# Performance work log

Measured on AMD Instinct MI355X. Metric: run time of the kernel, lower is better.

The kernel has to match this reference:

```python
import jax, jax.numpy as jnp
import numpy as np

HEADS = 8
NEG = -1e9
EPS = 1e-9


def setup_inputs() -> dict:
    key = jax.random.key(0)
    ks = jax.random.split(key, 24)
    N, D, E = 2048, 512, 64
    s = 0.02
    inp = {
        "xyz": jax.random.normal(ks[0], (N, 3), jnp.float32),
        "str_feat": jax.random.normal(ks[1], (N, D), jnp.float32),
        "esm_feat": jax.random.normal(ks[2], (N, E), jnp.float32),
        "y_hat": jax.random.uniform(ks[3], (N, 1), jnp.float32),
        "distance_mask": jax.random.randint(ks[4], (N, N), 0, 2, jnp.int32),
        "t": jnp.ones((1,), jnp.float32),
        "band_width": jnp.ones((1,), jnp.float32),
        "max_iter": 5,
        # main projections (torch Linear layout: y = x @ W.T + b)
        "Wq": jax.random.normal(ks[5], (D, D), jnp.float32) * s,
        "bq": jnp.zeros((D,), jnp.float32),
        "Wk": jax.random.normal(ks[6], (D, D), jnp.float32) * s,
        "bk": jnp.zeros((D,), jnp.float32),
        "Wv": jax.random.normal(ks[7], (D, D), jnp.float32) * s,
        "bv": jnp.zeros((D,), jnp.float32),
        "Wo": jax.random.normal(ks[8], (D, D), jnp.float32) * s,
        "bo": jnp.zeros((D,), jnp.float32),
        # esm projections (computed in the original forward but unused downstream)
        "Weq": jax.random.normal(ks[9], (E, E), jnp.float32) * s,
        "beq": jnp.zeros((E,), jnp.float32),
        "Wek": jax.random.normal(ks[10], (E, E), jnp.float32) * s,
        "bek": jnp.zeros((E,), jnp.float32),
        "Wev": jax.random.normal(ks[11], (E, E), jnp.float32) * s,
        "bev": jnp.zeros((E,), jnp.float32),
        "Weo": jax.random.normal(ks[12], (E, E), jnp.float32) * s,
        "beo": jnp.zeros((E,), jnp.float32),
    }
    return inp


def reference(xyz, str_feat, esm_feat, y_hat, distance_mask, t, band_width, max_iter,
              Wq, bq, Wk, bk, Wv, bv, Wo, bo,
              Weq, beq, Wek, bek, Wev, bev, Weo, beo):
    N, D = str_feat.shape
    h = HEADS
    dh = D // h

    q = str_feat @ Wq.T + bq
    k = str_feat @ Wk.T + bk
    v = str_feat @ Wv.T + bv
    # esm projections: computed in the original forward but never used (dead code; DCE'd under jit)
    _esm_q = esm_feat @ Weq.T + beq
    _esm_k = esm_feat @ Wek.T + bek
    _esm_v = esm_feat @ Wev.T + bev

    # [h, N, dh]
    qh = q.reshape(N, h, dh).transpose(1, 0, 2)
    kh = k.reshape(N, h, dh).transpose(1, 0, 2)
    vh = v.reshape(N, h, dh).transpose(1, 0, 2)

    scores = jnp.einsum('hnd,hmd->hnm', qh, kh) / jnp.sqrt(jnp.asarray(dh, qh.dtype))
    mask = (distance_mask > 0)[None]              # [1, N, N]
    yw = y_hat[:, 0][None, :]                     # [1, N] per-target weight
    inv_two_bw2 = 1.0 / (2.0 * band_width[0] ** 2)
    temp = t[0]

    def step(carry, _):
        xyz_c, _x = carry
        # squared pairwise distances via the expanded form (avoids [N,N,3])
        sq = jnp.sum(xyz_c * xyz_c, axis=-1)
        d2 = sq[:, None] + sq[None, :] - 2.0 * (xyz_c @ xyz_c.T)
        kern = jnp.exp(-d2 * inv_two_bw2)          # [N, N] band-width kernel
        logits = scores / temp + jnp.log(kern * yw + EPS)[None]
        logits = jnp.where(mask, logits, NEG)
        attn = jax.nn.softmax(logits, axis=-1)     # [h, N, N]
        xyz_new = jnp.einsum('nm,md->nd', attn.mean(0), xyz_c)  # mean-shift step
        x_new = jnp.einsum('hnm,hmd->hnd', attn, vh)            # [h, N, dh]
        return (xyz_new, x_new), None

    (xyz_out, xh), _ = jax.lax.scan(step, (xyz, jnp.zeros_like(vh)), None, length=max_iter)
    x = xh.transpose(1, 0, 2).reshape(N, D)
    out = x @ Wo.T + bo
    return xyz_out, out
```

## Files before the change

### kernel.cpp

```cpp
#include <hip/hip_runtime.h>


typedef __attribute__((ext_vector_type(8))) short bf16x8;
typedef __attribute__((ext_vector_type(4))) float f32x4;

__device__ __forceinline__ unsigned short f2bf(float f) {
    unsigned int u = __float_as_uint(f);
    u += 0x7fff + ((u >> 16) & 1);
    return (unsigned short)(u >> 16);
}
__device__ __forceinline__ float bf2f(unsigned short u) {
    return __uint_as_float((unsigned int)u << 16);
}

union EU { bf16x8 v; unsigned short u[8]; };

__global__ __launch_bounds__(256)
void conv_all(const float* __restrict__ strf,
              const float* __restrict__ Wq, const float* __restrict__ Wk,
              const float* __restrict__ Wv, const float* __restrict__ Wo,
              const int* __restrict__ dmask,
              unsigned short* __restrict__ sA, unsigned short* __restrict__ sW,
              unsigned char* __restrict__ mby)
{
    const long base = (long)(blockIdx.x * 256 + threadIdx.x) * 8;
    if (base >= 2097152) {
        const long rel = base - 2097152;
        int4 a = *reinterpret_cast<const int4*>(dmask + rel);
        int4 b = *reinterpret_cast<const int4*>(dmask + rel + 4);
        unsigned long long p = 0;
        p |= (a.x > 0) ? 0x01ULL : 0;  p |= (a.y > 0) ? 0x0100ULL : 0;
        p |= (a.z > 0) ? 0x010000ULL : 0;  p |= (a.w > 0) ? 0x01000000ULL : 0;
        p |= (b.x > 0) ? 0x0100000000ULL : 0;  p |= (b.y > 0) ? 0x010000000000ULL : 0;
        p |= (b.z > 0) ? 0x01000000000000ULL : 0;  p |= (b.w > 0) ? 0x0100000000000000ULL : 0;
        *reinterpret_cast<unsigned long long*>(mby + rel) = p;
        return;
    }
    const float* src;
    unsigned short* dst;
    if (base < 1048576) {
        src = strf + base; dst = sA + base;
    } else {
        const long rel = base - 1048576;
        const int seg = (int)(rel >> 18);
        const long off = rel & 262143;
        const float* Ws[4] = {Wq, Wk, Wv, Wo};
        src = Ws[seg] + off;
        dst = sW + (long)seg * 262144 + off;
    }
    float4 a = *reinterpret_cast<const float4*>(src);
    float4 b = *reinterpret_cast<const float4*>(src + 4);
    EU o;
    o.u[0] = f2bf(a.x); o.u[1] = f2bf(a.y); o.u[2] = f2bf(a.z); o.u[3] = f2bf(a.w);
    o.u[4] = f2bf(b.x); o.u[5] = f2bf(b.y); o.u[6] = f2bf(b.z); o.u[7] = f2bf(b.w);
    *reinterpret_cast<bf16x8*>(dst) = o.v;
}

__global__ __launch_bounds__(256)
void qkv_mfma(const unsigned short* __restrict__ sA,
              const unsigned short* __restrict__ sW,
              const float* __restrict__ bq, const float* __restrict__ bk,
              const float* __restrict__ bv,
              unsigned short* __restrict__ qh, unsigned short* __restrict__ kh,
              unsigned short* __restrict__ vT)
{
    const int z  = blockIdx.z;
    const int bx = blockIdx.x;
    const int by = blockIdx.y;
    const int tid = threadIdx.x;
    const int wv = tid >> 6;
    const int lane = tid & 63;
    const int row  = lane & 15;
    const int koct = (lane >> 4) * 8;
    const int n0 = bx * 64;

    const unsigned short* Ap = sA + (long)(n0 + wv * 16 + row) * 512;
    const unsigned short* Bp = sW + (long)z * 262144 + (long)(by * 64 + row) * 512;

    f32x4 acc[4] = {};
#pragma unroll
    for (int k0 = 0; k0 < 512; k0 += 32) {
        bf16x8 a = *reinterpret_cast<const bf16x8*>(Ap + k0 + koct);
#pragma unroll
        for (int t = 0; t < 4; t++) {
            bf16x8 b = *reinterpret_cast<const bf16x8*>(Bp + (long)(t * 16) * 512 + k0 + koct);
            acc[t] = __builtin_amdgcn_mfma_f32_16x16x32_bf16(a, b, acc[t], 0, 0, 0);
        }
    }

    if (z == 2) {
        const int rbase = n0 + wv * 16 + (lane >> 4) * 4;
#pragma unroll
        for (int t = 0; t < 4; t++) {
            const int d = by * 64 + t * 16 + (lane & 15);
            const float bb = bv[d];
            ushort4 o;
            o.x = f2bf(acc[t][0] + bb); o.y = f2bf(acc[t][1] + bb);
            o.z = f2bf(acc[t][2] + bb); o.w = f2bf(acc[t][3] + bb);
            *reinterpret_cast<ushort4*>(vT + (long)d * 2048 + rbase) = o;
        }
        return;
    }

    __shared__ float ls[64][68];
    const int lrb = wv * 16 + (lane >> 4) * 4;
    const int lcb = lane & 15;
#pragma unroll
    for (int t = 0; t < 4; t++)
#pragma unroll
        for (int r = 0; r < 4; r++)
            ls[lrb + r][t * 16 + lcb] = acc[t][r];
    __syncthreads();

    const float* bias = (z == 0) ? bq : bk;
    unsigned short* dst = (z == 0) ? qh : kh;
    const int r2 = tid >> 2;
    const int c2 = (tid & 3) * 16;
    float sv[16];
#pragma unroll
    for (int j = 0; j < 4; j++) {
        float4 s = *reinterpret_cast<const float4*>(&ls[r2][c2 + j * 4]);
        float4 bb = *reinterpret_cast<const float4*>(bias + by * 64 + c2 + j * 4);
        sv[j*4+0] = s.x + bb.x; sv[j*4+1] = s.y + bb.y;
        sv[j*4+2] = s.z + bb.z; sv[j*4+3] = s.w + bb.w;
    }
    EU o0, o1;
#pragma unroll
    for (int j = 0; j < 8; j++) { o0.u[j] = f2bf(sv[j]); o1.u[j] = f2bf(sv[8 + j]); }
    unsigned short* dp = dst + (long)(n0 + r2) * 512 + by * 64 + c2;
    *reinterpret_cast<bf16x8*>(dp)     = o0.v;
    *reinterpret_cast<bf16x8*>(dp + 8) = o1.v;
}

__global__ __launch_bounds__(256)
void scores_rows(const unsigned short* __restrict__ qh,
                 const unsigned short* __restrict__ kh,
                 const unsigned char* __restrict__ mby,
                 const float* __restrict__ tptr,
                 unsigned short* __restrict__ E2)
{
    const int h  = blockIdx.y;
    const int n0 = blockIdx.x * 16;
    const int tid = threadIdx.x;
    const int wv = tid >> 6;
    const int lane = tid & 63;
    const float scale = 1.0f / (8.0f * tptr[0]);

    __shared__ unsigned short lsb[4][16][260];

    const int arow = lane & 15;
    const int koct = (lane >> 4) * 8;
    const unsigned short* Aq = qh + (long)(n0 + arow) * 512 + h * 64;
    const bf16x8 aq0 = *reinterpret_cast<const bf16x8*>(Aq + koct);
    const bf16x8 aq1 = *reinterpret_cast<const bf16x8*>(Aq + 32 + koct);

    const int lr = (lane >> 4) * 4;
    const int lc = lane & 15;
    const int rlo = lane >> 5;
    const int cch = lane & 31;

#pragma unroll
    for (int half = 0; half < 2; half++) {
        const int mbase = wv * 512 + half * 256;
#pragma unroll
        for (int mt = 0; mt < 16; mt++) {
            const unsigned short* Bk = kh + (long)(mbase + mt * 16 + arow) * 512 + h * 64;
            bf16x8 b0 = *reinterpret_cast<const bf16x8*>(Bk + koct);
            bf16x8 b1 = *reinterpret_cast<const bf16x8*>(Bk + 32 + koct);
            f32x4 c = {};
            c = __builtin_amdgcn_mfma_f32_16x16x32_bf16(aq0, b0, c, 0, 0, 0);
            c = __builtin_amdgcn_mfma_f32_16x16x32_bf16(aq1, b1, c, 0, 0, 0);
#pragma unroll
            for (int r = 0; r < 4; r++)
                lsb[wv][lr + r][mt * 16 + lc] = f2bf(__expf(c[r] * scale));
        }
#pragma unroll
        for (int rp = 0; rp < 8; rp++) {
            const int row = rp * 2 + rlo;
            const int gn = n0 + row;
            const int m = mbase + cch * 8;
            EU e;
            e.v = *reinterpret_cast<const bf16x8*>(&lsb[wv][row][cch * 8]);
            unsigned long long mk =
                *reinterpret_cast<const unsigned long long*>(mby + (long)gn * 2048 + m);
            EU o;
#pragma unroll
            for (int j = 0; j < 8; j++)
                o.u[j] = ((mk >> (8 * j)) & 0xff) ? e.u[j] : (unsigned short)0;
            *reinterpret_cast<bf16x8*>(E2 + (long)gn * 16384 + h * 2048 + m) = o.v;
        }
    }
}

__global__ __launch_bounds__(256)
void ms_iter(const unsigned short* __restrict__ E2,
             const float* __restrict__ xyz_src,
             float* __restrict__ xyz_dst,
             const float* __restrict__ y_hat,
             const float* __restrict__ bwp,
             unsigned short* __restrict__ gbf,
             float* __restrict__ invzb,
             int wlast)
{
    const int n = blockIdx.x;
    const int tid = threadIdx.x;
    const int lane = tid & 63;
    const int wave = tid >> 6;
    const int m0 = tid * 8;

    __shared__ unsigned short Es[16384];
    __shared__ float red[64];

    {
        const unsigned short* gp = E2 + (long)n * 16384 + wave * 4096 + lane * 8;
#pragma unroll
        for (int c = 0; c < 8; c++) {
            __builtin_amdgcn_global_load_lds(
                (const __attribute__((address_space(1))) unsigned int*)(gp + c * 512),
                (__attribute__((address_space(3))) unsigned int*)&Es[wave * 4096 + c * 512],
                16, 0, 0);
        }
    }

    const float bw = bwp[0];
    const float c2k = 1.0f / (2.0f * bw * bw);
    const float xn = xyz_src[n * 3 + 0];
    const float yn = xyz_src[n * 3 + 1];
    const float zn = xyz_src[n * 3 + 2];
    const float sqn = xn * xn + yn * yn + zn * zn;

    float mx[8], my[8], mz[8];
    {
        const float4* xp = reinterpret_cast<const float4*>(xyz_src + (long)m0 * 3);
        float4 a = xp[0], b = xp[1], c = xp[2], d = xp[3], e = xp[4], f = xp[5];
        mx[0]=a.x; my[0]=a.y; mz[0]=a.z;  mx[1]=a.w; my[1]=b.x; mz[1]=b.y;
        mx[2]=b.z; my[2]=b.w; mz[2]=c.x;  mx[3]=c.y; my[3]=c.z; mz[3]=c.w;
        mx[4]=d.x; my[4]=d.y; mz[4]=d.z;  mx[5]=d.w; my[5]=e.x; mz[5]=e.y;
        mx[6]=e.z; my[6]=e.w; mz[6]=f.x;  mx[7]=f.y; my[7]=f.z; mz[7]=f.w;
    }
    float4 yh0 = *reinterpret_cast<const float4*>(y_hat + m0);
    float4 yh1 = *reinterpret_cast<const float4*>(y_hat + m0 + 4);
    float yh[8] = {yh0.x, yh0.y, yh0.z, yh0.w, yh1.x, yh1.y, yh1.z, yh1.w};

    float g[8];
#pragma unroll
    for (int j = 0; j < 8; j++) {
        const float d2 = sqn + (mx[j]*mx[j] + my[j]*my[j] + mz[j]*mz[j])
                       - 2.0f * (xn*mx[j] + yn*my[j] + zn*mz[j]);
        g[j] = __expf(-d2 * c2k) * yh[j] + 1e-9f;
    }

    __syncthreads();

    EU E[8];
#pragma unroll
    for (int h = 0; h < 8; h++)
        E[h].v = *reinterpret_cast<const bf16x8*>(&Es[h * 2048 + m0]);

    float z[8];
#pragma unroll
    for (int h = 0; h < 8; h++) {
        float zz = 0.f;
#pragma unroll
        for (int j = 0; j < 8; j++) zz += bf2f(E[h].u[j]) * g[j];
        z[h] = zz;
    }

#pragma unroll
    for (int h = 0; h < 8; h++) {
        float v = z[h];
#pragma unroll
        for (int off = 32; off > 0; off >>= 1) v += __shfl_down(v, off, 64);
        if (lane == 0) red[wave * 8 + h] = v;
    }
    __syncthreads();
    if (tid < 8) {
        const float s = red[tid] + red[8 + tid] + red[16 + tid] + red[24 + tid];
        const float iz = 1.0f / s;
        red[32 + tid] = iz;
        if (wlast) invzb[tid * 2048 + n] = iz;
    }
    __syncthreads();
    float invz[8];
#pragma unroll
    for (int h = 0; h < 8; h++) invz[h] = red[32 + h];

    float ax = 0.f, ay = 0.f, az = 0.f;
#pragma unroll
    for (int j = 0; j < 8; j++) {
        float w = 0.f;
#pragma unroll
        for (int h = 0; h < 8; h++) w += bf2f(E[h].u[j]) * invz[h];
        w *= 0.125f * g[j];
        ax += w * mx[j]; ay += w * my[j]; az += w * mz[j];
    }
    if (wlast) {
        EU og;
#pragma unroll
        for (int j = 0; j < 8; j++) og.u[j] = f2bf(g[j]);
        *reinterpret_cast<bf16x8*>(gbf + (long)n * 2048 + m0) = og.v;
    }

    float v3[3] = {ax, ay, az};
#pragma unroll
    for (int c = 0; c < 3; c++) {
        float v = v3[c];
#pragma unroll
        for (int off = 32; off > 0; off >>= 1) v += __shfl_down(v, off, 64);
        if (lane == 0) red[40 + c * 4 + wave] = v;
    }
    __syncthreads();
    if (tid < 3) {
        xyz_dst[n * 3 + tid] = red[40 + tid * 4 + 0] + red[40 + tid * 4 + 1] +
                               red[40 + tid * 4 + 2] + red[40 + tid * 4 + 3];
    }
}

__global__ __launch_bounds__(256)
void av_mfma(const unsigned short* __restrict__ E2,
             const unsigned short* __restrict__ gbf,
             const unsigned short* __restrict__ vT,
             float* __restrict__ P)
{
    const int h  = blockIdx.z;
    const int s  = blockIdx.y;
    const int bx = blockIdx.x;
    const int tid = threadIdx.x;
    const int wv = tid >> 6;
    const int lane = tid & 63;
    const int n0 = bx * 64;
    const int kc = s * 512;

    __shared__ unsigned short As[64][132];

    const int mrow = lane & 15;
    const int koct = (lane >> 4) * 8;
    const int srow = tid >> 4;
    const int skk  = (tid & 15) * 8;

    f32x4 acc[4] = {};
    for (int kt = 0; kt < 4; kt++) {
        const int kb = kc + kt * 128;
        __syncthreads();
#pragma unroll
        for (int l = 0; l < 4; l++) {
            const int row = l * 16 + srow;
            EU e, gg;
            e.v  = *reinterpret_cast<const bf16x8*>(E2 + (long)(n0 + row) * 16384 + h * 2048 + kb + skk);
            gg.v = *reinterpret_cast<const bf16x8*>(gbf + (long)(n0 + row) * 2048 + kb + skk);
            EU a;
#pragma unroll
            for (int j = 0; j < 8; j++)
                a.u[j] = f2bf(bf2f(e.u[j]) * bf2f(gg.u[j]));
            *reinterpret_cast<bf16x8*>(&As[row][skk]) = a.v;
        }
        __syncthreads();
#pragma unroll
        for (int k2 = 0; k2 < 128; k2 += 32) {
            bf16x8 a = *reinterpret_cast<const bf16x8*>(&As[wv * 16 + mrow][k2 + koct]);
#pragma unroll
            for (int t = 0; t < 4; t++) {
                bf16x8 b = *reinterpret_cast<const bf16x8*>(
                    vT + ((long)h * 64 + t * 16 + mrow) * 2048 + kb + k2 + koct);
                acc[t] = __builtin_amdgcn_mfma_f32_16x16x32_bf16(a, b, acc[t], 0, 0, 0);
            }
        }
    }

    float* Pp = P + (long)s * 1048576;
    const int rbase = n0 + wv * 16 + (lane >> 4) * 4;
    const int dcol = lane & 15;
#pragma unroll
    for (int t = 0; t < 4; t++)
#pragma unroll
        for (int r = 0; r < 4; r++)
            Pp[(long)(rbase + r) * 512 + h * 64 + t * 16 + dcol] = acc[t][r];
}

__global__ __launch_bounds__(256)
void out_mfma(const float* __restrict__ P,
              const float* __restrict__ invzb,
              const unsigned short* __restrict__ sW,
              const float* __restrict__ bo,
              float* __restrict__ out)
{
    const int bx = blockIdx.x;
    const int by = blockIdx.y;
    const int wv = threadIdx.x >> 6;
    const int lane = threadIdx.x & 63;
    const int row  = lane & 15;
    const int koct = (lane >> 4) * 8;
    const int n0 = bx * 64;
    const int n  = n0 + wv * 16 + row;

    const unsigned short* Bp = sW + 3L * 262144 + (long)(by * 64 + row) * 512;

    f32x4 acc[4] = {};
#pragma unroll
    for (int k0 = 0; k0 < 512; k0 += 32) {
        const int k = k0 + koct;
        float s[8] = {};
#pragma unroll
        for (int p = 0; p < 4; p++) {
            const float* pp = P + (long)p * 1048576 + (long)n * 512 + k;
            float4 x = *reinterpret_cast<const float4*>(pp);
            float4 y = *reinterpret_cast<const float4*>(pp + 4);
            s[0] += x.x; s[1] += x.y; s[2] += x.z; s[3] += x.w;
            s[4] += y.x; s[5] += y.y; s[6] += y.z; s[7] += y.w;
        }
        const float iz = invzb[(k >> 6) * 2048 + n];
        EU a;
#pragma unroll
        for (int j = 0; j < 8; j++) a.u[j] = f2bf(s[j] * iz);
#pragma unroll
        for (int t = 0; t < 4; t++) {
            bf16x8 b = *reinterpret_cast<const bf16x8*>(Bp + (long)(t * 16) * 512 + k0 + koct);
            acc[t] = __builtin_amdgcn_mfma_f32_16x16x32_bf16(a.v, b, acc[t], 0, 0, 0);
        }
    }

    const int rbase = n0 + wv * 16 + (lane >> 4) * 4;
    const int dcol = lane & 15;
#pragma unroll
    for (int t = 0; t < 4; t++) {
        const int col = by * 64 + t * 16 + dcol;
        const float bb = bo[col];
#pragma unroll
        for (int r = 0; r < 4; r++)
            out[(long)(rbase + r) * 512 + col] = acc[t][r] + bb;
    }
}

extern "C" void kernel_launch(void* const* d_in, const int* in_sizes, int n_in,
                              void* d_out, int out_size, void* d_ws, size_t ws_size,
                              hipStream_t stream)
{
    (void)in_sizes; (void)n_in; (void)out_size; (void)ws_size;

    const float* xyz   = (const float*)d_in[0];
    const float* strf  = (const float*)d_in[1];
    const float* yhat  = (const float*)d_in[3];
    const int*   dmask = (const int*)d_in[4];
    const float* tptr  = (const float*)d_in[5];
    const float* bwptr = (const float*)d_in[6];
    const float* Wq = (const float*)d_in[8];
    const float* bq = (const float*)d_in[9];
    const float* Wk = (const float*)d_in[10];
    const float* bk = (const float*)d_in[11];
    const float* Wv = (const float*)d_in[12];
    const float* bv = (const float*)d_in[13];
    const float* Wo = (const float*)d_in[14];
    const float* bo = (const float*)d_in[15];
    float* outp = (float*)d_out;

    char* wsb = (char*)d_ws;
    float* Ppart         = (float*)(wsb);
    unsigned short* sA   = (unsigned short*)(wsb + (18L << 20));
    unsigned short* sW   = (unsigned short*)(wsb + (20L << 20));
    unsigned short* qh   = (unsigned short*)(wsb + (22L << 20));
    unsigned short* kh   = (unsigned short*)(wsb + (24L << 20));
    unsigned short* vT   = (unsigned short*)(wsb + (26L << 20));
    float* xyzA          = (float*)(wsb + (28L << 20));
    float* xyzB          = xyzA + 8192;
    unsigned char* mby   = (unsigned char*)(wsb + (30L << 20));
    unsigned short* E2   = (unsigned short*)(wsb + (34L << 20));
    unsigned short* gbf  = (unsigned short*)(wsb + (98L << 20));
    float* invzb         = (float*)(wsb + (106L << 20));

    dim3 blk(256, 1, 1);

    conv_all<<<dim3(3072), blk, 0, stream>>>(strf, Wq, Wk, Wv, Wo, dmask, sA, sW, mby);
    qkv_mfma<<<dim3(32, 8, 3), blk, 0, stream>>>(sA, sW, bq, bk, bv, qh, kh, vT);

    scores_rows<<<dim3(128, 8), blk, 0, stream>>>(qh, kh, mby, tptr, E2);

    const float* src = xyz;
    float* dsts[5] = {xyzA, xyzB, xyzA, xyzB, outp};
    for (int it = 0; it < 5; it++) {
        ms_iter<<<dim3(2048), blk, 0, stream>>>(E2, src, dsts[it], yhat, bwptr,
                                                gbf, invzb, it == 4 ? 1 : 0);
        src = dsts[it];
    }

    av_mfma<<<dim3(32, 4, 8), blk, 0, stream>>>(E2, gbf, vT, Ppart);
    out_mfma<<<dim3(32, 8), blk, 0, stream>>>(Ppart, invzb, sW, bo, outp + 6144);
}
```

Baseline: 323.2 us.

## Fuse five mean-shift iterations into a persistent cooperative kernel with register-resident E

```diff
diff --git a/kernel.cpp b/kernel.cpp
--- a/kernel.cpp
+++ b/kernel.cpp
@@ -1,4 +1,7 @@
 #include <hip/hip_runtime.h>
+#include <hip/hip_cooperative_groups.h>
+
+namespace cg = cooperative_groups;
 
 
 typedef __attribute__((ext_vector_type(8))) short bf16x8;
@@ -192,127 +195,133 @@
     }
 }
 
-__global__ __launch_bounds__(256)
-void ms_iter(const unsigned short* __restrict__ E2,
-             const float* __restrict__ xyz_src,
-             float* __restrict__ xyz_dst,
-             const float* __restrict__ y_hat,
-             const float* __restrict__ bwp,
-             unsigned short* __restrict__ gbf,
-             float* __restrict__ invzb,
-             int wlast)
-{
-    const int n = blockIdx.x;
-    const int tid = threadIdx.x;
-    const int lane = tid & 63;
-    const int wave = tid >> 6;
-    const int m0 = tid * 8;
-
-    __shared__ unsigned short Es[16384];
-    __shared__ float red[64];
-
+__global__ __launch_bounds__(512, 2)
+void ms_persist(const unsigned short* __restrict__ E2,
+                const float* __restrict__ xyz0,
+                const float* __restrict__ y_hat,
+                const float* __restrict__ bwp,
+                float* __restrict__ xA, float* __restrict__ xB,
+                float* __restrict__ xC, float* __restrict__ xD,
+                float* __restrict__ xOut,
+                unsigned short* __restrict__ gbf,
+                float* __restrict__ invzb)
+{
+    cg::grid_group grid = cg::this_grid();
+    const int w = threadIdx.x >> 6;
+    const int lane = threadIdx.x & 63;
+    const int n = blockIdx.x * 8 + w;
+
+    EU Er[8][4];
     {
-        const unsigned short* gp = E2 + (long)n * 16384 + wave * 4096 + lane * 8;
-#pragma unroll
-        for (int c = 0; c < 8; c++) {
-            __builtin_amdgcn_global_load_lds(
-                (const __attribute__((address_space(1))) unsigned int*)(gp + c * 512),
-                (__attribute__((address_space(3))) unsigned int*)&Es[wave * 4096 + c * 512],
-                16, 0, 0);
-        }
+        const unsigned short* rowp = E2 + (long)n * 16384 + lane * 8;
+#pragma unroll
+        for (int h = 0; h < 8; h++)
+#pragma unroll
+            for (int c = 0; c < 4; c++)
+                Er[h][c].v = *reinterpret_cast<const bf16x8*>(rowp + h * 2048 + c * 512);
     }
 
     const float bw = bwp[0];
     const float c2k = 1.0f / (2.0f * bw * bw);
-    const float xn = xyz_src[n * 3 + 0];
-    const float yn = xyz_src[n * 3 + 1];
-    const float zn = xyz_src[n * 3 + 2];
-    const float sqn = xn * xn + yn * yn + zn * zn;
-
-    float mx[8], my[8], mz[8];
-    {
-        const float4* xp = reinterpret_cast<const float4*>(xyz_src + (long)m0 * 3);
-        float4 a = xp[0], b = xp[1], c = xp[2], d = xp[3], e = xp[4], f = xp[5];
-        mx[0]=a.x; my[0]=a.y; mz[0]=a.z;  mx[1]=a.w; my[1]=b.x; mz[1]=b.y;
-        mx[2]=b.z; my[2]=b.w; mz[2]=c.x;  mx[3]=c.y; my[3]=c.z; mz[3]=c.w;
-        mx[4]=d.x; my[4]=d.y; mz[4]=d.z;  mx[5]=d.w; my[5]=e.x; mz[5]=e.y;
-        mx[6]=e.z; my[6]=e.w; mz[6]=f.x;  mx[7]=f.y; my[7]=f.z; mz[7]=f.w;
-    }
-    float4 yh0 = *reinterpret_cast<const float4*>(y_hat + m0);
-    float4 yh1 = *reinterpret_cast<const float4*>(y_hat + m0 + 4);
-    float yh[8] = {yh0.x, yh0.y, yh0.z, yh0.w, yh1.x, yh1.y, yh1.z, yh1.w};
-
-    float g[8];
-#pragma unroll
-    for (int j = 0; j < 8; j++) {
-        const float d2 = sqn + (mx[j]*mx[j] + my[j]*my[j] + mz[j]*mz[j])
-                       - 2.0f * (xn*mx[j] + yn*my[j] + zn*mz[j]);
-        g[j] = __expf(-d2 * c2k) * yh[j] + 1e-9f;
-    }
-
-    __syncthreads();
-
-    EU E[8];
-#pragma unroll
-    for (int h = 0; h < 8; h++)
-        E[h].v = *reinterpret_cast<const bf16x8*>(&Es[h * 2048 + m0]);
-
-    float z[8];
-#pragma unroll
-    for (int h = 0; h < 8; h++) {
-        float zz = 0.f;
-#pragma unroll
-        for (int j = 0; j < 8; j++) zz += bf2f(E[h].u[j]) * g[j];
-        z[h] = zz;
-    }
-
-#pragma unroll
-    for (int h = 0; h < 8; h++) {
-        float v = z[h];
-#pragma unroll
-        for (int off = 32; off > 0; off >>= 1) v += __shfl_down(v, off, 64);
-        if (lane == 0) red[wave * 8 + h] = v;
-    }
-    __syncthreads();
-    if (tid < 8) {
-        const float s = red[tid] + red[8 + tid] + red[16 + tid] + red[24 + tid];
-        const float iz = 1.0f / s;
-        red[32 + tid] = iz;
-        if (wlast) invzb[tid * 2048 + n] = iz;
-    }
-    __syncthreads();
-    float invz[8];
-#pragma unroll
-    for (int h = 0; h < 8; h++) invz[h] = red[32 + h];
-
-    float ax = 0.f, ay = 0.f, az = 0.f;
-#pragma unroll
-    for (int j = 0; j < 8; j++) {
-        float w = 0.f;
-#pragma unroll
-        for (int h = 0; h < 8; h++) w += bf2f(E[h].u[j]) * invz[h];
-        w *= 0.125f * g[j];
-        ax += w * mx[j]; ay += w * my[j]; az += w * mz[j];
-    }
-    if (wlast) {
-        EU og;
-#pragma unroll
-        for (int j = 0; j < 8; j++) og.u[j] = f2bf(g[j]);
-        *reinterpret_cast<bf16x8*>(gbf + (long)n * 2048 + m0) = og.v;
-    }
-
-    float v3[3] = {ax, ay, az};
-#pragma unroll
-    for (int c = 0; c < 3; c++) {
-        float v = v3[c];
-#pragma unroll
-        for (int off = 32; off > 0; off >>= 1) v += __shfl_down(v, off, 64);
-        if (lane == 0) red[40 + c * 4 + wave] = v;
-    }
-    __syncthreads();
-    if (tid < 3) {
-        xyz_dst[n * 3 + tid] = red[40 + tid * 4 + 0] + red[40 + tid * 4 + 1] +
-                               red[40 + tid * 4 + 2] + red[40 + tid * 4 + 3];
+
+    const float* srcs[5] = {xyz0, xA, xB, xC, xD};
+    float* dsts[5] = {xA, xB, xC, xD, xOut};
+
+    for (int it = 0; it < 5; it++) {
+        const float* xs = srcs[it];
+        float* xd = dsts[it];
+        const int wlast = (it == 4);
+
+        const float xn = xs[n * 3 + 0];
+        const float yn = xs[n * 3 + 1];
+        const float zn = xs[n * 3 + 2];
+        const float sqn = xn * xn + yn * yn + zn * zn;
+
+        float g[32];
+#pragma unroll
+        for (int c = 0; c < 4; c++) {
+            const int mb = c * 512 + lane * 8;
+            const float4* xp = reinterpret_cast<const float4*>(xs + (long)mb * 3);
+            float4 a = xp[0], b = xp[1], cc = xp[2], d = xp[3], e = xp[4], f = xp[5];
+            float mx[8] = {a.x, a.w, b.z, cc.y, d.x, d.w, e.z, f.y};
+            float my[8] = {a.y, b.x, b.w, cc.z, d.y, e.x, e.w, f.z};
+            float mz[8] = {a.z, b.y, cc.x, cc.w, d.z, e.y, f.x, f.w};
+            float4 yh0 = *reinterpret_cast<const float4*>(y_hat + mb);
+            float4 yh1 = *reinterpret_cast<const float4*>(y_hat + mb + 4);
+            float yh[8] = {yh0.x, yh0.y, yh0.z, yh0.w, yh1.x, yh1.y, yh1.z, yh1.w};
+#pragma unroll
+            for (int j = 0; j < 8; j++) {
+                const float d2 = sqn + (mx[j]*mx[j] + my[j]*my[j] + mz[j]*mz[j])
+                               - 2.0f * (xn*mx[j] + yn*my[j] + zn*mz[j]);
+                g[c * 8 + j] = __expf(-d2 * c2k) * yh[j] + 1e-9f;
+            }
+        }
+
+        float zp[8] = {};
+#pragma unroll
+        for (int h = 0; h < 8; h++)
+#pragma unroll
+            for (int c = 0; c < 4; c++)
+#pragma unroll
+                for (int j = 0; j < 8; j++)
+                    zp[h] += bf2f(Er[h][c].u[j]) * g[c * 8 + j];
+
+#pragma unroll
+        for (int h = 0; h < 8; h++) {
+#pragma unroll
+            for (int off = 1; off < 64; off <<= 1)
+                zp[h] += __shfl_xor(zp[h], off, 64);
+        }
+        float iz[8];
+#pragma unroll
+        for (int h = 0; h < 8; h++) iz[h] = 1.0f / zp[h];
+        if (wlast && lane == 0) {
+#pragma unroll
+            for (int h = 0; h < 8; h++) invzb[h * 2048 + n] = iz[h];
+        }
+
+        float ax = 0.f, ay = 0.f, az = 0.f;
+#pragma unroll
+        for (int c = 0; c < 4; c++) {
+            const int mb = c * 512 + lane * 8;
+            const float4* xp = reinterpret_cast<const float4*>(xs + (long)mb * 3);
+            float4 a = xp[0], b = xp[1], cc = xp[2], d = xp[3], e = xp[4], f = xp[5];
+            float mx[8] = {a.x, a.w, b.z, cc.y, d.x, d.w, e.z, f.y};
+            float my[8] = {a.y, b.x, b.w, cc.z, d.y, e.x, e.w, f.z};
+            float mz[8] = {a.z, b.y, cc.x, cc.w, d.z, e.y, f.x, f.w};
+#pragma unroll
+            for (int j = 0; j < 8; j++) {
+                float wv = 0.f;
+#pragma unroll
+                for (int h = 0; h < 8; h++) wv += bf2f(Er[h][c].u[j]) * iz[h];
+                wv *= 0.125f * g[c * 8 + j];
+                ax += wv * mx[j]; ay += wv * my[j]; az += wv * mz[j];
+            }
+            if (wlast) {
+                EU og;
+#pragma unroll
+                for (int j = 0; j < 8; j++) og.u[j] = f2bf(g[c * 8 + j]);
+                *reinterpret_cast<bf16x8*>(gbf + (long)n * 2048 + mb) = og.v;
+            }
+        }
+
+        float v3[3] = {ax, ay, az};
+#pragma unroll
+        for (int cc2 = 0; cc2 < 3; cc2++) {
+#pragma unroll
+            for (int off = 32; off > 0; off >>= 1)
+                v3[cc2] += __shfl_down(v3[cc2], off, 64);
+        }
+        if (lane == 0) {
+            xd[n * 3 + 0] = v3[0];
+            xd[n * 3 + 1] = v3[1];
+            xd[n * 3 + 2] = v3[2];
+        }
+
+        if (it < 4) {
+            __threadfence();
+            grid.sync();
+        }
     }
 }
 
@@ -460,8 +469,10 @@
     unsigned short* qh   = (unsigned short*)(wsb + (22L << 20));
     unsigned short* kh   = (unsigned short*)(wsb + (24L << 20));
     unsigned short* vT   = (unsigned short*)(wsb + (26L << 20));
-    float* xyzA          = (float*)(wsb + (28L << 20));
-    float* xyzB          = xyzA + 8192;
+    float* xA            = (float*)(wsb + (28L << 20));
+    float* xB            = xA + 8192;
+    float* xC            = xA + 16384;
+    float* xD            = xA + 24576;
     unsigned char* mby   = (unsigned char*)(wsb + (30L << 20));
     unsigned short* E2   = (unsigned short*)(wsb + (34L << 20));
     unsigned short* gbf  = (unsigned short*)(wsb + (98L << 20));
@@ -471,15 +482,18 @@
 
     conv_all<<<dim3(3072), blk, 0, stream>>>(strf, Wq, Wk, Wv, Wo, dmask, sA, sW, mby);
     qkv_mfma<<<dim3(32, 8, 3), blk, 0, stream>>>(sA, sW, bq, bk, bv, qh, kh, vT);
-
     scores_rows<<<dim3(128, 8), blk, 0, stream>>>(qh, kh, mby, tptr, E2);
 
-    const float* src = xyz;
-    float* dsts[5] = {xyzA, xyzB, xyzA, xyzB, outp};
-    for (int it = 0; it < 5; it++) {
-        ms_iter<<<dim3(2048), blk, 0, stream>>>(E2, src, dsts[it], yhat, bwptr,
-                                                gbf, invzb, it == 4 ? 1 : 0);
-        src = dsts[it];
+    {
+        const unsigned short* E2c = E2;
+        float* xOut = outp;
+        void* kargs[] = {
+            (void*)&E2c, (void*)&xyz, (void*)&yhat, (void*)&bwptr,
+            (void*)&xA, (void*)&xB, (void*)&xC, (void*)&xD,
+            (void*)&xOut, (void*)&gbf, (void*)&invzb
+        };
+        hipLaunchCooperativeKernel((void*)ms_persist, dim3(256), dim3(512),
+                                   kargs, 0, stream);
     }
 
     av_mfma<<<dim3(32, 4, 8), blk, 0, stream>>>(E2, gbf, vT, Ppart);
```

New measurement: 1.047 ms. +224.0%, slower.
